# Optimization experiments

Hardware: AMD Instinct MI355X
Metric: run time of the kernel (lower is better)

The kernel has to match this reference:

```python
import jax, jax.numpy as jnp
import numpy as np

DIM = 768
NUM_HEADS = 16
D = DIM // NUM_HEADS  # 48


def setup_inputs() -> dict:
    key = jax.random.key(0)
    ks = jax.random.split(key, 7)
    x = jax.random.normal(ks[0], (4, 4096, DIM), dtype=jnp.float32)
    # Linear weights stored as [in, out] for x @ W + b
    s = 1.0 / np.sqrt(DIM)
    Wq = jax.random.uniform(ks[1], (DIM, D), jnp.float32, -s, s)
    Wk = jax.random.uniform(ks[2], (DIM, D), jnp.float32, -s, s)
    Wv = jax.random.uniform(ks[3], (DIM, D), jnp.float32, -s, s)
    bq = jax.random.uniform(ks[4], (D,), jnp.float32, -s, s)
    bk = jax.random.uniform(ks[5], (D,), jnp.float32, -s, s)
    bv = jax.random.uniform(ks[6], (D,), jnp.float32, -s, s)
    return {"x": x, "Wq": Wq, "bq": bq, "Wk": Wk, "bk": bk, "Wv": Wv, "bv": bv}


def reference(x, Wq, bq, Wk, bk, Wv, bv):
    # q, k, v: [B, S, D]
    q = x @ Wq + bq
    k = x @ Wk + bk
    v = x @ Wv + bv
    scale = 1.0 / jnp.sqrt(jnp.asarray(D, dtype=q.dtype))
    # scores: [B, S_q, S_k]
    scores = jnp.einsum("bqd,bkd->bqk", q, k) * scale
    # NOTE: softmax over dim=1 = the QUERY axis (faithful to original torch code)
    qk = jax.nn.softmax(scores, axis=1)
    # dropout is identity in eval mode (deterministic reference)
    attn = jnp.einsum("bqk,bkd->bqd", qk, v)
    return attn
```

## Files before the change

kernel.cpp:

```cpp
#include <hip/hip_runtime.h>
#include <hip/hip_bf16.h>

#define NB 4
#define SEQ 4096
#define CDIM 768
#define HD 48

typedef __attribute__((ext_vector_type(8))) __bf16 bf16x8;
typedef __attribute__((ext_vector_type(16))) float f32x16;

static constexpr float SCALE_LOG2E = 0.20823542135164923f;

__device__ __forceinline__ bf16x8 ldg8(const __hip_bfloat16* p) {
    uint4 u = *reinterpret_cast<const uint4*>(p);
    bf16x8 r;
    __builtin_memcpy(&r, &u, 16);
    return r;
}
__device__ __forceinline__ unsigned pk2(float lo, float hi) {
    const __hip_bfloat16 a = __float2bfloat16(lo);
    const __hip_bfloat16 b = __float2bfloat16(hi);
    unsigned short ua, ub;
    __builtin_memcpy(&ua, &a, 2);
    __builtin_memcpy(&ub, &b, 2);
    return (unsigned)ua | ((unsigned)ub << 16);
}
__device__ __forceinline__ bf16x8 mk8(unsigned w0, unsigned w1, unsigned w2, unsigned w3) {
    const uint4 u = make_uint4(w0, w1, w2, w3);
    bf16x8 r;
    __builtin_memcpy(&r, &u, 16);
    return r;
}
__device__ __forceinline__ void plswap(unsigned& a, unsigned& b) {
    asm volatile("v_permlane32_swap_b32 %0, %1" : "+v"(a), "+v"(b));
}
__device__ __forceinline__ size_t fragOff(int tile, int s, int h) {
    return (((size_t)tile * 3 + s) * 2 + h) * 256;
}
__device__ __forceinline__ void xcd_remap64(int id, int& b, int& st) {
    const int xcd = id & 7;
    b  = xcd >> 1;
    st = (xcd & 1) * 32 + (id >> 3);
}

__global__ __launch_bounds__(256) void prep_kernel(
    const float* __restrict__ Wq, const float* __restrict__ Wk,
    const float* __restrict__ Wv,
    const float* __restrict__ bq, const float* __restrict__ bk,
    const float* __restrict__ bv,
    __hip_bfloat16* __restrict__ Wf, float* __restrict__ bias)
{
    const int g = blockIdx.x * 256 + threadIdx.x;
    if (g < 15360) {
        const int rem  = g % 3072;
        const int nt   = g / 3072;
        const int ks   = rem >> 6;
        const int l2   = rem & 63;
        const int hh   = l2 >> 5;
        const int lane = l2 & 31;
        const int n    = nt * 32 + lane;
        const float* src = (n < 48) ? Wq : (n < 96) ? Wk : (n < 144) ? Wv : nullptr;
        const int col = (n < 48) ? n : (n < 96) ? (n - 48) : (n - 96);
        #pragma unroll
        for (int j = 0; j < 8; ++j) {
            const int k = ks * 16 + hh * 8 + j;
            const float wv = src ? src[(size_t)k * HD + col] : 0.0f;
            Wf[(size_t)g * 8 + j] = __float2bfloat16(wv);
        }
    }
    if (blockIdx.x == 0 && threadIdx.x < 160) {
        const int t = threadIdx.x;
        bias[t] = (t < 48) ? bq[t] : (t < 96) ? bk[t - 48] : (t < 144) ? bv[t - 96] : 0.0f;
    }
}

__global__ __launch_bounds__(320) void proj_kernel(
    const float* __restrict__ x,
    const __hip_bfloat16* __restrict__ Wf, const float* __restrict__ bias,
    __hip_bfloat16* __restrict__ Qf, __hip_bfloat16* __restrict__ Kf,
    float* __restrict__ Vf)
{
    __shared__ __hip_bfloat16 xs[2][24 * 512];

    const int t   = threadIdx.x;
    const int w   = t >> 6;
    const int l   = t & 63;
    const int lo5 = l & 31, h = l >> 5;
    const int mt  = blockIdx.x;
    const int m0  = mt * 32;

    const float* xb = x + (size_t)m0 * CDIM;
    #pragma unroll
    for (int i = 0; i < 10; ++i) {
        const int c = i * 320 + t;
        if (c < 3072) {
            const int r = c / 96, pos = c % 96;
            const float4 v = *reinterpret_cast<const float4*>(xb + (size_t)r * CDIM + pos * 4);
            const int ksl = pos >> 2, hh = (pos >> 1) & 1, j = (pos & 1) * 4;
            *reinterpret_cast<uint2*>(&xs[0][ksl * 512 + (hh * 32 + r) * 8 + j]) =
                make_uint2(pk2(v.x, v.y), pk2(v.z, v.w));
        }
    }
    float4 stg[10];
    #pragma unroll
    for (int i = 0; i < 10; ++i) {
        const int c = i * 320 + t;
        if (c < 3072) {
            const int r = c / 96, pos = c % 96;
            stg[i] = *reinterpret_cast<const float4*>(xb + (size_t)r * CDIM + 384 + pos * 4);
        }
    }
    __syncthreads();

    const __hip_bfloat16* bp = Wf + (size_t)w * 24576 + l * 8;
    f32x16 acc = {};
    #pragma unroll 8
    for (int ks = 0; ks < 24; ++ks) {
        bf16x8 a;
        __builtin_memcpy(&a, &xs[0][ks * 512 + l * 8], 16);
        const bf16x8 b = ldg8(bp + (size_t)ks * 512);
        acc = __builtin_amdgcn_mfma_f32_32x32x16_bf16(a, b, acc, 0, 0, 0);
    }

    #pragma unroll
    for (int i = 0; i < 10; ++i) {
        const int c = i * 320 + t;
        if (c < 3072) {
            const int r = c / 96, pos = c % 96;
            const int ksl = pos >> 2, hh = (pos >> 1) & 1, j = (pos & 1) * 4;
            *reinterpret_cast<uint2*>(&xs[1][ksl * 512 + (hh * 32 + r) * 8 + j]) =
                make_uint2(pk2(stg[i].x, stg[i].y), pk2(stg[i].z, stg[i].w));
        }
    }
    __syncthreads();
    #pragma unroll 8
    for (int ks = 0; ks < 24; ++ks) {
        bf16x8 a;
        __builtin_memcpy(&a, &xs[1][ks * 512 + l * 8], 16);
        const bf16x8 b = ldg8(bp + (size_t)(24 + ks) * 512);
        acc = __builtin_amdgcn_mfma_f32_32x32x16_bf16(a, b, acc, 0, 0, 0);
    }

    const int n_g = w * 32 + lo5;
    const float bs = bias[n_g];
    if (n_g < 96) {
        const bool isQ = (n_g < 48);
        const int d  = isQ ? n_g : n_g - 48;
        const int s  = d >> 4;
        const int hf = (d >> 3) & 1;
        __hip_bfloat16* base = (isQ ? Qf : Kf) + fragOff(mt, s, hf) + (d & 7);
        #pragma unroll
        for (int r = 0; r < 16; ++r) {
            const int mrow = (r & 3) + 8 * (r >> 2) + 4 * h;
            float val = acc[r] + bs;
            if (isQ) val *= SCALE_LOG2E;
            base[mrow * 8] = __float2bfloat16(val);
        }
    } else if (n_g < 144) {
        const int d = n_g - 96;
        #pragma unroll
        for (int r = 0; r < 16; ++r) {
            const int m = m0 + (r & 3) + 8 * (r >> 2) + 4 * h;
            Vf[(size_t)m * HD + d] = acc[r] + bs;
        }
    }
}

__global__ __launch_bounds__(512, 2) void stats_kernel(
    const __hip_bfloat16* __restrict__ Qf, const __hip_bfloat16* __restrict__ Kf,
    const float* __restrict__ Vf, __hip_bfloat16* __restrict__ Vt)
{
    __shared__ float part[8][64];
    __shared__ float linv[64];

    const int t   = threadIdx.x;
    const int w   = t >> 6;
    const int l   = t & 63;
    const int lo5 = l & 31, h = l >> 5;
    int b, kst;
    xcd_remap64(blockIdx.x, b, kst);
    const int ktile0 = b * 128 + kst * 2;

    bf16x8 ka[6];
    #pragma unroll
    for (int s = 0; s < 3; ++s) {
        ka[s]     = ldg8(Kf + fragOff(ktile0,     s, h) + lo5 * 8);
        ka[3 + s] = ldg8(Kf + fragOff(ktile0 + 1, s, h) + lo5 * 8);
    }

    float lsum[32];
    #pragma unroll
    for (int r = 0; r < 32; ++r) lsum[r] = 0.0f;

    const int qt0 = b * 128 + w * 16;
    bf16x8 qb[2][3];
    #pragma unroll
    for (int s = 0; s < 3; ++s)
        qb[0][s] = ldg8(Qf + fragOff(qt0, s, h) + lo5 * 8);

    #pragma unroll
    for (int qq = 0; qq < 16; ++qq) {
        const int cur = qq & 1;
        if (qq < 15) {
            #pragma unroll
            for (int s = 0; s < 3; ++s)
                qb[cur ^ 1][s] = ldg8(Qf + fragOff(qt0 + qq + 1, s, h) + lo5 * 8);
        }
        f32x16 a0 = {}, a1 = {};
        __builtin_amdgcn_s_setprio(1);
        #pragma unroll
        for (int s = 0; s < 3; ++s)
            a0 = __builtin_amdgcn_mfma_f32_32x32x16_bf16(ka[s], qb[cur][s], a0, 0, 0, 0);
        #pragma unroll
        for (int s = 0; s < 3; ++s)
            a1 = __builtin_amdgcn_mfma_f32_32x32x16_bf16(ka[3 + s], qb[cur][s], a1, 0, 0, 0);
        __builtin_amdgcn_s_setprio(0);
        #pragma unroll
        for (int r = 0; r < 16; ++r) {
            lsum[r]      += __builtin_amdgcn_exp2f(a0[r]);
            lsum[16 + r] += __builtin_amdgcn_exp2f(a1[r]);
        }
    }

    #pragma unroll
    for (int r = 0; r < 32; ++r) {
        lsum[r] += __shfl_xor(lsum[r], 1);
        lsum[r] += __shfl_xor(lsum[r], 2);
        lsum[r] += __shfl_xor(lsum[r], 4);
        lsum[r] += __shfl_xor(lsum[r], 8);
        lsum[r] += __shfl_xor(lsum[r], 16);
    }
    if (lo5 == 0) {
        #pragma unroll
        for (int r = 0; r < 16; ++r) {
            const int row = (r & 3) + 8 * (r >> 2) + 4 * h;
            part[w][row]      = lsum[r];
            part[w][32 + row] = lsum[16 + r];
        }
    }
    __syncthreads();
    if (t < 64) {
        float s = 0.0f;
        #pragma unroll
        for (int p = 0; p < 8; ++p) s += part[p][t];
        linv[t] = 1.0f / s;
    }
    __syncthreads();

    const int kp = t & 15;
    const int dg = t >> 4;
    #pragma unroll
    for (int tt = 0; tt < 2; ++tt) {
        const int ktile = ktile0 + tt;
        const float f0 = linv[tt * 32 + 2 * kp], f1 = linv[tt * 32 + 2 * kp + 1];
        __hip_bfloat16* vtb = Vt + (size_t)ktile * 2048;
        const float* vfb = Vf + ((size_t)b * SEQ + (kst * 2 + tt) * 32 + 2 * kp) * HD;
        {
            const int d = dg;
            const float v0 = vfb[d], v1 = vfb[HD + d];
            *reinterpret_cast<unsigned*>(&vtb[d * 32 + 2 * kp]) = pk2(v0 * f0, v1 * f1);
        }
        if (dg < 16) {
            const int d = dg + 32;
            const float v0 = vfb[d], v1 = vfb[HD + d];
            *reinterpret_cast<unsigned*>(&vtb[d * 32 + 2 * kp]) = pk2(v0 * f0, v1 * f1);
        }
    }
}

__global__ __launch_bounds__(512, 2) void pv_kernel(
    const __hip_bfloat16* __restrict__ Qf, const __hip_bfloat16* __restrict__ Kf,
    const __hip_bfloat16* __restrict__ Vt, float* __restrict__ out)
{
    __shared__ float red[8][32][64];

    const int t   = threadIdx.x;
    const int w   = t >> 6;
    const int l   = t & 63;
    const int lo5 = l & 31, h = l >> 5;
    int b, qst;
    xcd_remap64(blockIdx.x, b, qst);
    const int qtile0 = b * 128 + qst * 2;
    const int q0     = qst * 64;

    bf16x8 qb[6];
    #pragma unroll
    for (int s = 0; s < 3; ++s) {
        qb[s]     = ldg8(Qf + fragOff(qtile0,     s, h) + lo5 * 8);
        qb[3 + s] = ldg8(Qf + fragOff(qtile0 + 1, s, h) + lo5 * 8);
    }

    f32x16 o00 = {}, o01 = {}, o10 = {}, o11 = {};
    const int kt0 = b * 128 + w * 16;

    bf16x8 ka[2][3], vv[2][4];
    {
        #pragma unroll
        for (int s = 0; s < 3; ++s)
            ka[0][s] = ldg8(Kf + fragOff(kt0, s, h) + lo5 * 8);
        const __hip_bfloat16* vt = Vt + (size_t)kt0 * 2048 + lo5 * 32 + 8 * h;
        vv[0][0] = ldg8(vt);
        vv[0][1] = ldg8(vt + 16);
        vv[0][2] = ldg8(vt + 1024);
        vv[0][3] = ldg8(vt + 1024 + 16);
    }

    #pragma unroll
    for (int kk = 0; kk < 16; ++kk) {
        const int cur = kk & 1;
        if (kk < 15) {
            const int ktn = kt0 + kk + 1;
            #pragma unroll
            for (int s = 0; s < 3; ++s)
                ka[cur ^ 1][s] = ldg8(Kf + fragOff(ktn, s, h) + lo5 * 8);
            const __hip_bfloat16* vtn = Vt + (size_t)ktn * 2048 + lo5 * 32 + 8 * h;
            vv[cur ^ 1][0] = ldg8(vtn);
            vv[cur ^ 1][1] = ldg8(vtn + 16);
            vv[cur ^ 1][2] = ldg8(vtn + 1024);
            vv[cur ^ 1][3] = ldg8(vtn + 1024 + 16);
        }

        #pragma unroll
        for (int qt = 0; qt < 2; ++qt) {
            f32x16 acc = {};
            __builtin_amdgcn_s_setprio(1);
            #pragma unroll
            for (int s = 0; s < 3; ++s)
                acc = __builtin_amdgcn_mfma_f32_32x32x16_bf16(
                    ka[cur][s], qb[3 * qt + s], acc, 0, 0, 0);
            __builtin_amdgcn_s_setprio(0);

            float p[16];
            #pragma unroll
            for (int r = 0; r < 16; ++r) p[r] = __builtin_amdgcn_exp2f(acc[r]);

            unsigned w0 = pk2(p[0],  p[1]),  w1 = pk2(p[2],  p[3]);
            unsigned w2 = pk2(p[4],  p[5]),  w3 = pk2(p[6],  p[7]);
            unsigned w4 = pk2(p[8],  p[9]),  w5 = pk2(p[10], p[11]);
            unsigned w6 = pk2(p[12], p[13]), w7 = pk2(p[14], p[15]);
            plswap(w0, w2);
            plswap(w1, w3);
            plswap(w4, w6);
            plswap(w5, w7);
            const bf16x8 pa0 = mk8(w0, w1, w2, w3);
            const bf16x8 pa1 = mk8(w4, w5, w6, w7);

            __builtin_amdgcn_s_setprio(1);
            if (qt == 0) {
                o00 = __builtin_amdgcn_mfma_f32_32x32x16_bf16(pa0, vv[cur][0], o00, 0, 0, 0);
                o00 = __builtin_amdgcn_mfma_f32_32x32x16_bf16(pa1, vv[cur][1], o00, 0, 0, 0);
                o01 = __builtin_amdgcn_mfma_f32_32x32x16_bf16(pa0, vv[cur][2], o01, 0, 0, 0);
                o01 = __builtin_amdgcn_mfma_f32_32x32x16_bf16(pa1, vv[cur][3], o01, 0, 0, 0);
            } else {
                o10 = __builtin_amdgcn_mfma_f32_32x32x16_bf16(pa0, vv[cur][0], o10, 0, 0, 0);
                o10 = __builtin_amdgcn_mfma_f32_32x32x16_bf16(pa1, vv[cur][1], o10, 0, 0, 0);
                o11 = __builtin_amdgcn_mfma_f32_32x32x16_bf16(pa0, vv[cur][2], o11, 0, 0, 0);
                o11 = __builtin_amdgcn_mfma_f32_32x32x16_bf16(pa1, vv[cur][3], o11, 0, 0, 0);
            }
            __builtin_amdgcn_s_setprio(0);
        }
    }

    #pragma unroll
    for (int round = 0; round < 2; ++round) {
        const f32x16& a = round ? o10 : o00;
        const f32x16& c = round ? o11 : o01;
        #pragma unroll
        for (int r = 0; r < 16; ++r) {
            red[w][r][l]      = a[r];
            red[w][16 + r][l] = c[r];
        }
        __syncthreads();
        {
            const int rr = t >> 4;
            const int l0 = (t & 15) * 4;
            float4 s = make_float4(0.f, 0.f, 0.f, 0.f);
            #pragma unroll
            for (int p = 0; p < 8; ++p) {
                const float4 v = *reinterpret_cast<const float4*>(&red[p][rr][l0]);
                s.x += v.x; s.y += v.y; s.z += v.z; s.w += v.w;
            }
            const int r    = rr & 15;
            const int row  = (r & 3) + 8 * (r >> 2) + 4 * (l0 >> 5);
            const int qrow = q0 + round * 32 + row;
            if (rr < 16) {
                *reinterpret_cast<float4*>(
                    &out[((size_t)(b * SEQ) + qrow) * HD + (l0 & 31)]) = s;
            } else if ((l0 & 31) < 16) {
                *reinterpret_cast<float4*>(
                    &out[((size_t)(b * SEQ) + qrow) * HD + 32 + (l0 & 31)]) = s;
            }
        }
        __syncthreads();
    }
}

extern "C" void kernel_launch(void* const* d_in, const int* in_sizes, int n_in,
                              void* d_out, int out_size, void* d_ws, size_t ws_size,
                              hipStream_t stream)
{
    const float* x  = (const float*)d_in[0];
    const float* Wq = (const float*)d_in[1];
    const float* bq = (const float*)d_in[2];
    const float* Wk = (const float*)d_in[3];
    const float* bk = (const float*)d_in[4];
    const float* Wv = (const float*)d_in[5];
    const float* bv = (const float*)d_in[6];
    float* out = (float*)d_out;

    const size_t FRAG = (size_t)512 * 6 * 256;
    __hip_bfloat16* Qf  = (__hip_bfloat16*)d_ws;
    __hip_bfloat16* Kf  = Qf + FRAG;
    float*          Vf  = (float*)(Kf + FRAG);
    __hip_bfloat16* Vt  = (__hip_bfloat16*)(Vf + (size_t)NB * SEQ * HD);
    __hip_bfloat16* Wf  = Vt + (size_t)NB * 128 * 2048;
    float*          bias = (float*)(Wf + (size_t)5 * 48 * 512);

    prep_kernel<<<dim3(60), 256, 0, stream>>>(Wq, Wk, Wv, bq, bk, bv, Wf, bias);
    proj_kernel<<<dim3(512), 320, 0, stream>>>(x, Wf, bias, Qf, Kf, Vf);
    stats_kernel<<<dim3(256), 512, 0, stream>>>(Qf, Kf, Vf, Vt);
    pv_kernel<<<dim3(256), 512, 0, stream>>>(Qf, Kf, Vt, out);
}
```

Measured before the change: 77.48 us.

## Load full x tile at once in projection, add MFMA priority, relax launch bounds

The projection kernel now converts the whole 32x768 x tile into a single shared buffer in one pass, replacing the two-half staged scheme that overlapped the second half's global loads with the first half's MFMAs. The MFMA loop raises wave priority around each MFMA with s_setprio. Separately, the stats and pv kernels drop the min-blocks-per-CU hint of 2, letting the compiler use more registers at the risk of lower occupancy.

```diff
diff --git a/kernel.cpp b/kernel.cpp
--- a/kernel.cpp
+++ b/kernel.cpp
@@ -80,7 +80,7 @@
     __hip_bfloat16* __restrict__ Qf, __hip_bfloat16* __restrict__ Kf,
     float* __restrict__ Vf)
 {
-    __shared__ __hip_bfloat16 xs[2][24 * 512];
+    __shared__ __hip_bfloat16 xs[48 * 512];
 
     const int t   = threadIdx.x;
     const int w   = t >> 6;
@@ -91,23 +91,16 @@
 
     const float* xb = x + (size_t)m0 * CDIM;
     #pragma unroll
-    for (int i = 0; i < 10; ++i) {
+    for (int i = 0; i < 20; ++i) {
         const int c = i * 320 + t;
-        if (c < 3072) {
-            const int r = c / 96, pos = c % 96;
-            const float4 v = *reinterpret_cast<const float4*>(xb + (size_t)r * CDIM + pos * 4);
-            const int ksl = pos >> 2, hh = (pos >> 1) & 1, j = (pos & 1) * 4;
-            *reinterpret_cast<uint2*>(&xs[0][ksl * 512 + (hh * 32 + r) * 8 + j]) =
-                make_uint2(pk2(v.x, v.y), pk2(v.z, v.w));
-        }
-    }
-    float4 stg[10];
-    #pragma unroll
-    for (int i = 0; i < 10; ++i) {
-        const int c = i * 320 + t;
-        if (c < 3072) {
-            const int r = c / 96, pos = c % 96;
-            stg[i] = *reinterpret_cast<const float4*>(xb + (size_t)r * CDIM + 384 + pos * 4);
+        if (c < 6144) {
+            const int r   = c / 192;
+            const int pos = c % 192;
+            const int k   = pos * 4;
+            const float4 v = *reinterpret_cast<const float4*>(xb + (size_t)r * CDIM + k);
+            const int ks = k >> 4, hh = (k >> 3) & 1, j = k & 7;
+            const uint2 d = make_uint2(pk2(v.x, v.y), pk2(v.z, v.w));
+            *reinterpret_cast<uint2*>(&xs[ks * 512 + (hh * 32 + r) * 8 + j]) = d;
         }
     }
     __syncthreads();
@@ -115,30 +108,13 @@
     const __hip_bfloat16* bp = Wf + (size_t)w * 24576 + l * 8;
     f32x16 acc = {};
     #pragma unroll 8
-    for (int ks = 0; ks < 24; ++ks) {
+    for (int ks = 0; ks < 48; ++ks) {
         bf16x8 a;
-        __builtin_memcpy(&a, &xs[0][ks * 512 + l * 8], 16);
+        __builtin_memcpy(&a, &xs[ks * 512 + l * 8], 16);
         const bf16x8 b = ldg8(bp + (size_t)ks * 512);
+        __builtin_amdgcn_s_setprio(1);
         acc = __builtin_amdgcn_mfma_f32_32x32x16_bf16(a, b, acc, 0, 0, 0);
-    }
-
-    #pragma unroll
-    for (int i = 0; i < 10; ++i) {
-        const int c = i * 320 + t;
-        if (c < 3072) {
-            const int r = c / 96, pos = c % 96;
-            const int ksl = pos >> 2, hh = (pos >> 1) & 1, j = (pos & 1) * 4;
-            *reinterpret_cast<uint2*>(&xs[1][ksl * 512 + (hh * 32 + r) * 8 + j]) =
-                make_uint2(pk2(stg[i].x, stg[i].y), pk2(stg[i].z, stg[i].w));
-        }
-    }
-    __syncthreads();
-    #pragma unroll 8
-    for (int ks = 0; ks < 24; ++ks) {
-        bf16x8 a;
-        __builtin_memcpy(&a, &xs[1][ks * 512 + l * 8], 16);
-        const bf16x8 b = ldg8(bp + (size_t)(24 + ks) * 512);
-        acc = __builtin_amdgcn_mfma_f32_32x32x16_bf16(a, b, acc, 0, 0, 0);
+        __builtin_amdgcn_s_setprio(0);
     }
 
     const int n_g = w * 32 + lo5;
@@ -166,7 +142,7 @@
     }
 }
 
-__global__ __launch_bounds__(512, 2) void stats_kernel(
+__global__ __launch_bounds__(512) void stats_kernel(
     const __hip_bfloat16* __restrict__ Qf, const __hip_bfloat16* __restrict__ Kf,
     const float* __restrict__ Vf, __hip_bfloat16* __restrict__ Vt)
 {
@@ -268,7 +244,7 @@
     }
 }
 
-__global__ __launch_bounds__(512, 2) void pv_kernel(
+__global__ __launch_bounds__(512) void pv_kernel(
     const __hip_bfloat16* __restrict__ Qf, const __hip_bfloat16* __restrict__ Kf,
     const __hip_bfloat16* __restrict__ Vt, float* __restrict__ out)
 {
```

Result: slower. 83.59 us (+7.9%).
